# Performance work log

Hardware: AMD Instinct MI355X
Metric: run time of the kernel (lower is better)

Reference implementation:

```python
import jax, jax.numpy as jnp
import numpy as np

BIT = 8  # weight quantization bits (module init arg)

def quantize(w, bit):
    # symmetric uniform quantization to `bit` bits (Quant from source repo)
    qmax = 2.0 ** (bit - 1) - 1.0
    scale = jnp.max(jnp.abs(w)) / qmax
    return jnp.round(w / scale) * scale


def setup_inputs() -> dict:
    key = jax.random.key(0)
    k1, k2, k3 = jax.random.split(key, 3)
    signal = jax.random.normal(k1, (16, 64, 16384), dtype=jnp.float32)  # [B, Cin, L]
    weight = jax.random.normal(k2, (64, 64, 128), dtype=jnp.float32)    # [Cout, Cin, K]
    bias = jax.random.normal(k3, (64,), dtype=jnp.float32)
    return {"signal": signal, "weight": weight, "bias": bias}


def reference(signal, weight, bias):
    # padding=0, stride=1, dilation=1, groups=1 (init kwargs), so the kron
    # dilation expansion and signal padding are identities.
    w = quantize(weight, BIT)
    B, Cin, L = signal.shape
    Cout, _, K = w.shape
    L_even = L + (L % 2)  # source pads signal to even length along last dim
    sig = jnp.pad(signal, ((0, 0), (0, 0), (0, L_even - L)))
    ker = jnp.pad(w, ((0, 0), (0, 0), (0, L_even - K)))  # zero-pad kernel to signal length
    sig_fr = jnp.fft.rfft(sig, axis=-1)                   # [B, Cin, F]
    ker_fr = jnp.conj(jnp.fft.rfft(ker, axis=-1))         # kernel_fr.imag *= -1 -> conj, [Cout, Cin, F]
    # complex_matmul with groups=1: contract over input channels per frequency bin
    out_fr = jnp.einsum('bif,oif->bof', sig_fr, ker_fr)   # [B, Cout, F]
    out = jnp.fft.irfft(out_fr, n=L_even, axis=-1)        # [B, Cout, L_even]
    out = out[:, :, : L - K + 1]                          # crop to valid conv output, stride 1
    return out + bias[None, :, None]
```

## Files before the change

kernel.cpp:

```cpp
#include <hip/hip_runtime.h>

typedef unsigned short ushort_t;
typedef unsigned int   uint_t;
typedef signed char    i8_t;

using int32x4  = __attribute__((ext_vector_type(4))) int;
using int32x16 = __attribute__((ext_vector_type(16))) int;

#define BATCH 16
#define CIN   64
#define COUT  64
#define LSIG  16384
#define KW    128
#define LOUT  (LSIG - KW + 1)

#define NTILE 512
#define ROWS  640

__global__ void k_amax_part(const float* __restrict__ x, float* __restrict__ part, int n4) {
  const float4* x4 = (const float4*)x;
  float m = 0.f;
  for (int i = blockIdx.x * blockDim.x + threadIdx.x; i < n4; i += gridDim.x * blockDim.x) {
    float4 v = x4[i];
    m = fmaxf(m, fmaxf(fmaxf(fabsf(v.x), fabsf(v.y)), fmaxf(fabsf(v.z), fabsf(v.w))));
  }
  for (int off = 32; off > 0; off >>= 1) m = fmaxf(m, __shfl_down(m, off, 64));
  __shared__ float sm[4];
  if ((threadIdx.x & 63) == 0) sm[threadIdx.x >> 6] = m;
  __syncthreads();
  if (threadIdx.x == 0)
    part[blockIdx.x] = fmaxf(fmaxf(sm[0], sm[1]), fmaxf(sm[2], sm[3]));
}

__global__ void k_amax_fin(const float* __restrict__ part, float* __restrict__ scales) {
  const int t = threadIdx.x;
  float mw = (t < 64) ? part[t] : 0.f;
  float ms = 0.f;
  for (int i = t; i < 512; i += 256) ms = fmaxf(ms, part[64 + i]);
  for (int off = 32; off > 0; off >>= 1) {
    mw = fmaxf(mw, __shfl_down(mw, off, 64));
    ms = fmaxf(ms, __shfl_down(ms, off, 64));
  }
  __shared__ float sw[4], ss[4];
  if ((t & 63) == 0) { sw[t >> 6] = mw; ss[t >> 6] = ms; }
  __syncthreads();
  if (t == 0) {
    scales[0] = fmaxf(fmaxf(sw[0], sw[1]), fmaxf(sw[2], sw[3]));
    scales[1] = fmaxf(fmaxf(ss[0], ss[1]), fmaxf(ss[2], ss[3]));
  }
}

__global__ void k_wprep(const float* __restrict__ w, const float* __restrict__ scales,
                        i8_t* __restrict__ wt3) {
  const float scale = scales[0] / 127.0f;
  const int k = blockIdx.x;
  const int t = threadIdx.x;
  const int frag = t >> 6, lane = t & 63;
  const int hi = lane >> 5, l31 = lane & 31;
  const int of = frag >> 1, ks = frag & 1;
  const int o = of * 32 + l31;
  const int ibase = ks * 32 + hi * 16;
  union { i8_t b[16]; uint4 u; } pk;
#pragma unroll
  for (int j = 0; j < 16; ++j) {
    const float q = rintf(w[((size_t)o * CIN + ibase + j) * KW + k] / scale);
    pk.b[j] = (i8_t)q;
  }
  *(uint4*)(wt3 + (((size_t)k * 4 + frag) * 64 + lane) * 16) = pk.u;
}

__global__ void k_sprep(const float* __restrict__ sig, const float* __restrict__ scales,
                        uint4* __restrict__ sigT8) {
  __shared__ float tile[64][65];
  const float rs = 127.0f / scales[1];
  const int b = blockIdx.y;
  const int n0 = blockIdx.x * 64;
  const int t = threadIdx.x;
  {
    const int i = t >> 2, q = t & 3;
    const float4* src = (const float4*)(sig + ((size_t)(b * CIN + i)) * LSIG + n0 + q * 16);
    float4 v0 = src[0], v1 = src[1], v2 = src[2], v3 = src[3];
    float* trow = &tile[i][q * 16];
    trow[0]=v0.x; trow[1]=v0.y; trow[2]=v0.z;  trow[3]=v0.w;
    trow[4]=v1.x; trow[5]=v1.y; trow[6]=v1.z;  trow[7]=v1.w;
    trow[8]=v2.x; trow[9]=v2.y; trow[10]=v2.z; trow[11]=v2.w;
    trow[12]=v3.x; trow[13]=v3.y; trow[14]=v3.z; trow[15]=v3.w;
  }
  __syncthreads();
  const int nl = t >> 2, cg = t & 3;
  const int n = n0 + nl;
  const int cbase = (cg ^ ((n >> 1) & 3)) * 16;
  uint_t u[4];
#pragma unroll
  for (int d = 0; d < 4; ++d) {
    uint_t word = 0;
#pragma unroll
    for (int e = 0; e < 4; ++e) {
      float q = rintf(tile[cbase + d * 4 + e][nl] * rs);
      q = fminf(127.0f, fmaxf(-127.0f, q));
      word |= ((uint_t)(unsigned char)(i8_t)(int)q) << (8 * e);
    }
    u[d] = word;
  }
  sigT8[((size_t)b * LSIG + n) * 4 + cg] = make_uint4(u[0], u[1], u[2], u[3]);
}

#define KS_I8(T, KS, BCUR, BNXT) do {                                                  \
    { const int rb_ = rowbase + (T) + 1;                                               \
      _Pragma("unroll") for (int nf = 0; nf < 4; ++nf) {                               \
        const int r_ = rb_ + nf * 32;                                                  \
        const int slot_ = (((KS) * 2 + hi) ^ ((r_ >> 1) & 3));                         \
        BNXT[KS][nf] = *(const int32x4*)(lds8 + r_ * 64 + slot_ * 16);                 \
      } }                                                                              \
    __builtin_amdgcn_sched_barrier(0);                                                 \
    __builtin_amdgcn_s_setprio(1);                                                     \
    _Pragma("unroll") for (int of = 0; of < 2; ++of)                                   \
      _Pragma("unroll") for (int nf = 0; nf < 4; ++nf)                                 \
        acc[of][nf] = __builtin_amdgcn_mfma_i32_32x32x32_i8(A[of * 2 + (KS)], BCUR[KS][nf], acc[of][nf], 0, 0, 0); \
    __builtin_amdgcn_s_setprio(0);                                                     \
    __builtin_amdgcn_sched_barrier(0);                                                 \
    { const char* pa_ = wa3 + (size_t)((T) + 1) * 4096;                                \
      _Pragma("unroll") for (int of = 0; of < 2; ++of)                                 \
        A[of * 2 + (KS)] = *(const int32x4*)(pa_ + (of * 2 + (KS)) * 1024);            \
    }                                                                                  \
    __builtin_amdgcn_sched_barrier(0);                                                 \
  } while (0)

__global__ __launch_bounds__(256, 2) void k_conv(
    const uint4* __restrict__ sigT8, const i8_t* __restrict__ wt3,
    const float* __restrict__ scales, const float* __restrict__ bias,
    float* __restrict__ out)
{
  __shared__ __align__(16) i8_t lds8[ROWS * 64];
  const int b  = blockIdx.y;
  const int n0 = blockIdx.x * NTILE;
  const int t  = threadIdx.x;
  const int wv = t >> 6;
  const int lane = t & 63;
  const int l31 = lane & 31, hi = lane >> 5;

  {
    const size_t base = ((size_t)b * LSIG + n0) * 4;
    const size_t lim  = (size_t)BATCH * LSIG * 4;
    uint4* dst = (uint4*)lds8;
    for (int c = t; c < ROWS * 4; c += 256) {
      size_t g = base + c;
      if (g >= lim) g = lim - 1;
      dst[c] = sigT8[g];
    }
  }
  __syncthreads();

  int32x16 acc[2][4];
#pragma unroll
  for (int i = 0; i < 2; ++i)
#pragma unroll
    for (int j = 0; j < 4; ++j)
#pragma unroll
      for (int r = 0; r < 16; ++r) acc[i][j][r] = 0;

  const char* wa3 = (const char*)wt3 + (size_t)lane * 16;
  const int rowbase = wv * 128 + l31;

  int32x4 A[4], BbE[2][4], BbO[2][4];
#pragma unroll
  for (int f = 0; f < 4; ++f) A[f] = *(const int32x4*)(wa3 + f * 1024);
#pragma unroll
  for (int ks = 0; ks < 2; ++ks)
#pragma unroll
    for (int nf = 0; nf < 4; ++nf) {
      const int r_ = rowbase + nf * 32;
      const int slot_ = ((ks * 2 + hi) ^ ((r_ >> 1) & 3));
      BbE[ks][nf] = *(const int32x4*)(lds8 + r_ * 64 + slot_ * 16);
    }

  for (int tp = 0; tp < KW; tp += 2) {
    KS_I8(tp,     0, BbE, BbO);
    KS_I8(tp,     1, BbE, BbO);
    KS_I8(tp + 1, 0, BbO, BbE);
    KS_I8(tp + 1, 1, BbO, BbE);
  }

  const float sc = (scales[0] / 127.0f) * (scales[1] / 127.0f);
#pragma unroll
  for (int of = 0; of < 2; ++of) {
#pragma unroll
    for (int nf = 0; nf < 4; ++nf) {
      const int n = n0 + wv * 128 + nf * 32 + l31;
      if (n < LOUT) {
#pragma unroll
        for (int r = 0; r < 16; ++r) {
          const int o = of * 32 + 4 * hi + (r & 3) + 8 * (r >> 2);
          out[((size_t)b * COUT + o) * LOUT + n] = (float)acc[of][nf][r] * sc + bias[o];
        }
      }
    }
  }
}

extern "C" void kernel_launch(void* const* d_in, const int* in_sizes, int n_in,
                              void* d_out, int out_size, void* d_ws, size_t ws_size,
                              hipStream_t stream) {
  const float* sig  = (const float*)d_in[0];
  const float* w    = (const float*)d_in[1];
  const float* bias = (const float*)d_in[2];
  float* out = (float*)d_out;

  float* scales = (float*)d_ws;
  float* part   = (float*)((char*)d_ws + 64);
  i8_t*  wt3    = (i8_t*)((char*)d_ws + 4096);
  uint4* sigT8  = (uint4*)((char*)d_ws + (size_t)(2u << 20));

  hipLaunchKernelGGL(k_amax_part, dim3(64),  dim3(256), 0, stream, w,   part,      COUT * CIN * KW / 4);
  hipLaunchKernelGGL(k_amax_part, dim3(512), dim3(256), 0, stream, sig, part + 64, BATCH * CIN * LSIG / 4);
  hipLaunchKernelGGL(k_amax_fin,  dim3(1),   dim3(256), 0, stream, (const float*)part, scales);
  hipLaunchKernelGGL(k_wprep, dim3(KW), dim3(256), 0, stream, w, (const float*)scales, wt3);
  hipLaunchKernelGGL(k_sprep, dim3(LSIG / 64, BATCH), dim3(256), 0, stream, sig, (const float*)scales, sigT8);
  hipLaunchKernelGGL(k_conv, dim3((LOUT + NTILE - 1) / NTILE, BATCH), dim3(256), 0, stream,
                     sigT8, wt3, (const float*)scales, bias, out);
}
```

Baseline: 160.0 us.

## Read int8 signal operands directly from global planes instead of staging in LDS

The quantized signal is stored in four channel-group planes so that each lane's 16-byte B fragment for a given tap is a contiguous, coalesced global load. The conv kernel drops the LDS staging buffer, its fill loop and the barrier, and loads B fragments straight from global/L2. The per-k-slice sched_barrier interleaving is also replaced by a per-tap macro that issues all eight MFMAs together. The intent is to cut LDS traffic and the fill latency and to free LDS for occupancy, at the cost of more global/L2 load pressure. Rows read near the end of a batch row fall into the next batch's region or past the end of a plane, where the old code clamped the index.

After: 202.4 us. 1.27x slower.

```diff
diff --git a/kernel.cpp b/kernel.cpp
--- a/kernel.cpp
+++ b/kernel.cpp
@@ -15,7 +15,7 @@
 #define LOUT  (LSIG - KW + 1)
 
 #define NTILE 512
-#define ROWS  640
+#define PLANE_B ((size_t)BATCH * LSIG * 16)
 
 __global__ void k_amax_part(const float* __restrict__ x, float* __restrict__ part, int n4) {
   const float4* x4 = (const float4*)x;
@@ -70,7 +70,7 @@
 }
 
 __global__ void k_sprep(const float* __restrict__ sig, const float* __restrict__ scales,
-                        uint4* __restrict__ sigT8) {
+                        uint4* __restrict__ sigT8c) {
   __shared__ float tile[64][65];
   const float rs = 127.0f / scales[1];
   const int b = blockIdx.y;
@@ -87,9 +87,9 @@
     trow[12]=v3.x; trow[13]=v3.y; trow[14]=v3.z; trow[15]=v3.w;
   }
   __syncthreads();
-  const int nl = t >> 2, cg = t & 3;
+  const int nl = t & 63, cg = t >> 6;
   const int n = n0 + nl;
-  const int cbase = (cg ^ ((n >> 1) & 3)) * 16;
+  const int cbase = cg * 16;
   uint_t u[4];
 #pragma unroll
   for (int d = 0; d < 4; ++d) {
@@ -102,36 +102,32 @@
     }
     u[d] = word;
   }
-  sigT8[((size_t)b * LSIG + n) * 4 + cg] = make_uint4(u[0], u[1], u[2], u[3]);
-}
-
-#define KS_I8(T, KS, BCUR, BNXT) do {                                                  \
-    { const int rb_ = rowbase + (T) + 1;                                               \
+  sigT8c[(size_t)cg * (BATCH * LSIG) + (size_t)b * LSIG + n] = make_uint4(u[0], u[1], u[2], u[3]);
+}
+
+#define TAP_I8(T, BC, BN) do {                                                         \
+    { const char* q0_ = pB0 + ((T) + 1) * 16;                                          \
+      const char* q1_ = pB1 + ((T) + 1) * 16;                                          \
       _Pragma("unroll") for (int nf = 0; nf < 4; ++nf) {                               \
-        const int r_ = rb_ + nf * 32;                                                  \
-        const int slot_ = (((KS) * 2 + hi) ^ ((r_ >> 1) & 3));                         \
-        BNXT[KS][nf] = *(const int32x4*)(lds8 + r_ * 64 + slot_ * 16);                 \
+        BN[0][nf] = *(const int32x4*)(q0_ + nf * 512);                                 \
+        BN[1][nf] = *(const int32x4*)(q1_ + nf * 512);                                 \
       } }                                                                              \
-    __builtin_amdgcn_sched_barrier(0);                                                 \
     __builtin_amdgcn_s_setprio(1);                                                     \
-    _Pragma("unroll") for (int of = 0; of < 2; ++of)                                   \
-      _Pragma("unroll") for (int nf = 0; nf < 4; ++nf)                                 \
-        acc[of][nf] = __builtin_amdgcn_mfma_i32_32x32x32_i8(A[of * 2 + (KS)], BCUR[KS][nf], acc[of][nf], 0, 0, 0); \
+    _Pragma("unroll") for (int ks = 0; ks < 2; ++ks)                                   \
+      _Pragma("unroll") for (int of = 0; of < 2; ++of)                                 \
+        _Pragma("unroll") for (int nf = 0; nf < 4; ++nf)                               \
+          acc[of][nf] = __builtin_amdgcn_mfma_i32_32x32x32_i8(A[of * 2 + ks], BC[ks][nf], acc[of][nf], 0, 0, 0); \
     __builtin_amdgcn_s_setprio(0);                                                     \
-    __builtin_amdgcn_sched_barrier(0);                                                 \
-    { const char* pa_ = wa3 + (size_t)((T) + 1) * 4096;                                \
-      _Pragma("unroll") for (int of = 0; of < 2; ++of)                                 \
-        A[of * 2 + (KS)] = *(const int32x4*)(pa_ + (of * 2 + (KS)) * 1024);            \
-    }                                                                                  \
-    __builtin_amdgcn_sched_barrier(0);                                                 \
+    { const char* pa_ = wa3 + ((size_t)((T) + 1)) * 4096;                              \
+      _Pragma("unroll") for (int f = 0; f < 4; ++f)                                    \
+        A[f] = *(const int32x4*)(pa_ + f * 1024); }                                    \
   } while (0)
 
 __global__ __launch_bounds__(256, 2) void k_conv(
-    const uint4* __restrict__ sigT8, const i8_t* __restrict__ wt3,
+    const char* __restrict__ sigT8c, const i8_t* __restrict__ wt3,
     const float* __restrict__ scales, const float* __restrict__ bias,
     float* __restrict__ out)
 {
-  __shared__ __align__(16) i8_t lds8[ROWS * 64];
   const int b  = blockIdx.y;
   const int n0 = blockIdx.x * NTILE;
   const int t  = threadIdx.x;
@@ -139,18 +135,6 @@
   const int lane = t & 63;
   const int l31 = lane & 31, hi = lane >> 5;
 
-  {
-    const size_t base = ((size_t)b * LSIG + n0) * 4;
-    const size_t lim  = (size_t)BATCH * LSIG * 4;
-    uint4* dst = (uint4*)lds8;
-    for (int c = t; c < ROWS * 4; c += 256) {
-      size_t g = base + c;
-      if (g >= lim) g = lim - 1;
-      dst[c] = sigT8[g];
-    }
-  }
-  __syncthreads();
-
   int32x16 acc[2][4];
 #pragma unroll
   for (int i = 0; i < 2; ++i)
@@ -162,23 +146,22 @@
   const char* wa3 = (const char*)wt3 + (size_t)lane * 16;
   const int rowbase = wv * 128 + l31;
 
+  const size_t row0 = (size_t)b * LSIG + n0 + rowbase;
+  const char* pB0 = sigT8c + (size_t)(0 * 2 + hi) * PLANE_B + row0 * 16;
+  const char* pB1 = sigT8c + (size_t)(1 * 2 + hi) * PLANE_B + row0 * 16;
+
   int32x4 A[4], BbE[2][4], BbO[2][4];
 #pragma unroll
   for (int f = 0; f < 4; ++f) A[f] = *(const int32x4*)(wa3 + f * 1024);
 #pragma unroll
-  for (int ks = 0; ks < 2; ++ks)
-#pragma unroll
-    for (int nf = 0; nf < 4; ++nf) {
-      const int r_ = rowbase + nf * 32;
-      const int slot_ = ((ks * 2 + hi) ^ ((r_ >> 1) & 3));
-      BbE[ks][nf] = *(const int32x4*)(lds8 + r_ * 64 + slot_ * 16);
-    }
+  for (int nf = 0; nf < 4; ++nf) {
+    BbE[0][nf] = *(const int32x4*)(pB0 + nf * 512);
+    BbE[1][nf] = *(const int32x4*)(pB1 + nf * 512);
+  }
 
   for (int tp = 0; tp < KW; tp += 2) {
-    KS_I8(tp,     0, BbE, BbO);
-    KS_I8(tp,     1, BbE, BbO);
-    KS_I8(tp + 1, 0, BbO, BbE);
-    KS_I8(tp + 1, 1, BbO, BbE);
+    TAP_I8(tp,     BbE, BbO);
+    TAP_I8(tp + 1, BbO, BbE);
   }
 
   const float sc = (scales[0] / 127.0f) * (scales[1] / 127.0f);
@@ -209,13 +192,14 @@
   float* scales = (float*)d_ws;
   float* part   = (float*)((char*)d_ws + 64);
   i8_t*  wt3    = (i8_t*)((char*)d_ws + 4096);
-  uint4* sigT8  = (uint4*)((char*)d_ws + (size_t)(2u << 20));
+  char*  sigT8c = (char*)d_ws + (size_t)(2u << 20);
 
   hipLaunchKernelGGL(k_amax_part, dim3(64),  dim3(256), 0, stream, w,   part,      COUT * CIN * KW / 4);
   hipLaunchKernelGGL(k_amax_part, dim3(512), dim3(256), 0, stream, sig, part + 64, BATCH * CIN * LSIG / 4);
   hipLaunchKernelGGL(k_amax_fin,  dim3(1),   dim3(256), 0, stream, (const float*)part, scales);
   hipLaunchKernelGGL(k_wprep, dim3(KW), dim3(256), 0, stream, w, (const float*)scales, wt3);
-  hipLaunchKernelGGL(k_sprep, dim3(LSIG / 64, BATCH), dim3(256), 0, stream, sig, (const float*)scales, sigT8);
+  hipLaunchKernelGGL(k_sprep, dim3(LSIG / 64, BATCH), dim3(256), 0, stream, sig, (const float*)scales,
+                     (uint4*)sigT8c);
   hipLaunchKernelGGL(k_conv, dim3((LOUT + NTILE - 1) / NTILE, BATCH), dim3(256), 0, stream,
-                     sigT8, wt3, (const float*)scales, bias, out);
-}
+                     sigT8c, wt3, (const float*)scales, bias, out);
+}
```
